# Kernel tuning notes

Hardware: AMD Instinct MI355X
Metric: run time of the kernel (lower is better)

The kernel has to match this reference:

```python
import jax, jax.numpy as jnp
import numpy as np

HEADS = 16
KV_HEADS = 4
DIM_HEAD = 64
DIM = 1024
B, N = 2, 2048


def setup_inputs() -> dict:
    key = jax.random.key(0)
    k1, k2, k3 = jax.random.split(key, 3)
    x = jax.random.normal(k1, (B, N, DIM), dtype=jnp.float32)
    Wq = jax.random.normal(k2, (DIM, HEADS * DIM_HEAD), dtype=jnp.float32) / np.sqrt(DIM)
    Wkv = jax.random.normal(k3, (DIM, 2 * KV_HEADS * DIM_HEAD), dtype=jnp.float32) / np.sqrt(DIM)
    k_scale = jnp.ones((HEADS, 1, DIM_HEAD), dtype=jnp.float32)
    return {"x": x, "Wq": Wq, "Wkv": Wkv, "k_scale": k_scale}


def reference(x, Wq, Wkv, k_scale):
    b, n, _ = x.shape
    g = HEADS // KV_HEADS  # query heads per kv head
    scale = DIM_HEAD ** -0.5
    # fused qkv projections (no bias)
    q = (x @ Wq).reshape(b, n, HEADS, DIM_HEAD)
    kv = x @ Wkv
    k, v = jnp.split(kv, 2, axis=-1)
    k = k.reshape(b, n, KV_HEADS, DIM_HEAD).transpose(0, 2, 1, 3)  # b k n d
    v = v.reshape(b, n, KV_HEADS, DIM_HEAD).transpose(0, 2, 1, 3)  # b k n d
    # group query heads: b, kv_heads, g, n, d
    qg = q.transpose(0, 2, 1, 3).reshape(b, KV_HEADS, g, n, DIM_HEAD)
    # per-query-head k scale, applied to the group-broadcast k (qk-norm)
    ks = k_scale.reshape(KV_HEADS, g, 1, DIM_HEAD)
    kk = k[:, :, None, :, :] * ks  # b k g n d
    dots = jnp.einsum('bkgid,bkgjd->bkgij', qg, kk) * scale
    attn = jax.nn.softmax(dots, axis=-1)
    out = jnp.einsum('bkgij,bkjd->bkgid', attn, v)  # v broadcast over g
    out = out.reshape(b, HEADS, n, DIM_HEAD).transpose(0, 2, 1, 3).reshape(b, n, HEADS * DIM_HEAD)
    return out
```

## Files before the change

kernel.cpp:

```cpp
#include <hip/hip_runtime.h>
#include <stdint.h>
#include <math.h>

typedef __attribute__((ext_vector_type(8))) __bf16 bf16x8;
typedef __attribute__((ext_vector_type(4))) float f32x4;
typedef __attribute__((ext_vector_type(16))) float f32x16;

__device__ __forceinline__ uint32_t f32_to_bf16_rne(float f) {
  union { float f; uint32_t u; } v; v.f = f;
  return (v.u + 0x7FFFu + ((v.u >> 16) & 1u)) >> 16;
}

__device__ __forceinline__ uint32_t cvt_pk_bf16(float lo, float hi) {
  uint32_t r;
  asm("v_cvt_pk_bf16_f32 %0, %1, %2" : "=v"(r) : "v"(lo), "v"(hi));
  return r;
}

__device__ __forceinline__ void gld16(void* lds, const void* g) {
  __builtin_amdgcn_global_load_lds(
      (__attribute__((address_space(1))) void*)(g),
      (__attribute__((address_space(3))) void*)(lds), 16, 0, 0);
}

__device__ __forceinline__ f32x4 mfma16(bf16x8 a, bf16x8 b, f32x4 c) {
  return __builtin_amdgcn_mfma_f32_16x16x32_bf16(a, b, c, 0, 0, 0);
}
__device__ __forceinline__ f32x16 mfma32(bf16x8 a, bf16x8 b, f32x16 c) {
  return __builtin_amdgcn_mfma_f32_32x32x16_bf16(a, b, c, 0, 0, 0);
}

#define LOG2E 1.44269504088896340736f

__global__ __launch_bounds__(256) void k_convert(const float* __restrict__ x,
                                                 const float* __restrict__ wq,
                                                 const float* __restrict__ wkv,
                                                 uint16_t* __restrict__ xb,
                                                 uint16_t* __restrict__ wt) {
  __shared__ float tile[64][65];
  int blk = blockIdx.x;
  int t = threadIdx.x;
  if (blk < 2048) {
    int i = blk * 256 + t;
    const float4* xv = (const float4*)x;
    float4 a = xv[2 * i], b2 = xv[2 * i + 1];
    uint32_t w0 = f32_to_bf16_rne(a.x) | (f32_to_bf16_rne(a.y) << 16);
    uint32_t w1 = f32_to_bf16_rne(a.z) | (f32_to_bf16_rne(a.w) << 16);
    uint32_t w2 = f32_to_bf16_rne(b2.x) | (f32_to_bf16_rne(b2.y) << 16);
    uint32_t w3 = f32_to_bf16_rne(b2.z) | (f32_to_bf16_rne(b2.w) << 16);
    ((uint4*)xb)[i] = make_uint4(w0, w1, w2, w3);
  } else {
    int blk2 = blk - 2048;
    int c0 = (blk2 % 24) * 64, k0 = (blk2 / 24) * 64;
    int col = t & 63, rq = t >> 6;
#pragma unroll
    for (int rr = 0; rr < 16; rr++) {
      int r = rr * 4 + rq;
      int c = c0 + col;
      float v = (c < 1024) ? wq[(uint64_t)(k0 + r) * 1024 + c]
                           : wkv[(uint64_t)(k0 + r) * 512 + (c - 1024)];
      tile[r][col] = v;
    }
    __syncthreads();
#pragma unroll
    for (int rr = 0; rr < 16; rr++) {
      int a = rr * 4 + rq;
      wt[(uint64_t)(c0 + a) * 1024 + k0 + col] = (uint16_t)f32_to_bf16_rne(tile[col][a]);
    }
  }
}

__global__ __launch_bounds__(256, 3) void k_proj_gemm(
    const uint16_t* __restrict__ xb, const uint16_t* __restrict__ wt,
    const float* __restrict__ kscale, uint16_t* __restrict__ q_ws,
    uint16_t* __restrict__ kf_ws, uint16_t* __restrict__ vf_ws) {
  __shared__ __align__(16) uint16_t ring[2][12288];
  int t = threadIdx.x;
  int w = t >> 6, l = t & 63;
  int lq = l & 15, lg = l >> 4;
  int id = blockIdx.x;
  int xcd = id & 7, idx = id >> 3;
  int rrp = idx & 3, cc = idx >> 2;
  int m0 = (xcd * 4 + rrp) * 128, n0 = cc * 64;
  int wr = w >> 1, wc = w & 1;
  f32x4 acc[4][2] = {};

  auto stage = [&](int slot, int k0) {
#pragma unroll
    for (int j = 0; j < 4; j++) {
      int c = j * 256 + t;
      int r = c >> 3, s = c & 7;
      int sl = s ^ (r & 7);
      gld16((char*)&ring[slot][0] + c * 16,
            xb + (uint64_t)(m0 + r) * 1024 + k0 + sl * 8);
    }
#pragma unroll
    for (int j = 0; j < 2; j++) {
      int c = j * 256 + t;
      int r = c >> 3, s = c & 7;
      int sl = s ^ (r & 7);
      gld16((char*)&ring[slot][8192] + c * 16,
            wt + (uint64_t)(n0 + r) * 1024 + k0 + sl * 8);
    }
  };

  stage(0, 0);
  asm volatile("s_waitcnt vmcnt(0)" ::: "memory");
  __builtin_amdgcn_s_barrier();

  int cur = 0;
  for (int it = 0; it < 16; ++it) {
    if (it + 1 < 16) stage(cur ^ 1, (it + 1) * 64);

    const uint16_t* As = &ring[cur][0];
    const uint16_t* Bs = &ring[cur][8192];
    bf16x8 af[2][4], bfr[2][2];
#pragma unroll
    for (int kk = 0; kk < 2; kk++) {
#pragma unroll
      for (int m = 0; m < 4; m++) {
        int r = wr * 64 + m * 16 + lq;
        int sl = (kk * 4 + lg) ^ (r & 7);
        af[kk][m] = *(const bf16x8*)(As + r * 64 + sl * 8);
      }
#pragma unroll
      for (int n = 0; n < 2; n++) {
        int r = wc * 32 + n * 16 + lq;
        int sl = (kk * 4 + lg) ^ (r & 7);
        bfr[kk][n] = *(const bf16x8*)(Bs + r * 64 + sl * 8);
      }
    }
    __builtin_amdgcn_s_setprio(1);
#pragma unroll
    for (int kk = 0; kk < 2; kk++)
#pragma unroll
      for (int m = 0; m < 4; m++)
#pragma unroll
        for (int n = 0; n < 2; n++)
          acc[m][n] = mfma16(af[kk][m], bfr[kk][n], acc[m][n]);
    __builtin_amdgcn_s_setprio(0);

    asm volatile("s_waitcnt vmcnt(0) lgkmcnt(0)" ::: "memory");
    __builtin_amdgcn_s_barrier();
    cur ^= 1;
  }

#pragma unroll
  for (int m = 0; m < 4; m++)
#pragma unroll
    for (int n = 0; n < 2; n++)
#pragma unroll
      for (int jj = 0; jj < 4; jj++) {
        int row = m0 + wr * 64 + m * 16 + 4 * lg + jj;
        int col = n0 + wc * 32 + n * 16 + lq;
        float val = acc[m][n][jj];
        int b = row >> 11, nn = row & 2047;
        if (col < 1024) {
          val *= kscale[col] * 0.125f * LOG2E;
          q_ws[((uint64_t)((b * 16 + (col >> 6)) * 2048 + nn)) * 64 + (col & 63)] =
              (uint16_t)f32_to_bf16_rne(val);
        } else if (col < 1280) {
          int kvh = (col - 1024) >> 6;
          int d = col & 63;
          int gsu = nn >> 5, lrr = nn & 31;
          int mm = d >> 4, hh = (d >> 3) & 1, el = d & 7;
          kf_ws[(uint64_t)(b * 4 + kvh) * 131072 +
                (uint64_t)((((gsu * 4 + mm) * 64) + hh * 32 + lrr) * 8 + el)] =
              (uint16_t)f32_to_bf16_rne(val);
        } else {
          int kvh = (col - 1280) >> 6;
          int d = col & 63;
          int gsu = nn >> 5, jj2 = (nn >> 4) & 1, hh = (nn >> 3) & 1, el = nn & 7;
          int dd = d >> 5, lrr = d & 31;
          vf_ws[(uint64_t)(b * 4 + kvh) * 131072 +
                (uint64_t)((((gsu * 4 + dd * 2 + jj2) * 64) + hh * 32 + lrr) * 8 + el)] =
              (uint16_t)f32_to_bf16_rne(val);
        }
      }
}

__global__ __launch_bounds__(512, 1) void k_attn(const uint16_t* __restrict__ q_ws,
                                                 const uint16_t* __restrict__ kf_ws,
                                                 const uint16_t* __restrict__ vf_ws,
                                                 float* __restrict__ out) {
  extern __shared__ __align__(16) char smem[];

  int t = threadIdx.x, w = t >> 6, l = t & 63;
  int lr = l & 31, hi = l >> 5;
  int qg = w & 3, half = w >> 2;
  int blk = blockIdx.x;
  int c = blk & 7, j = blk >> 3;
  int b = c >> 2, kvh = c & 3;
  int h = kvh * 4 + (j >> 3), qb = j & 7;

  const uint16_t* Qb = q_ws + (uint64_t)(b * 16 + h) * 2048 * 64;
  const uint16_t* Kb = kf_ws + (uint64_t)(b * 4 + kvh) * 131072;
  const uint16_t* Vb = vf_ws + (uint64_t)(b * 4 + kvh) * 131072;
  int qrow0 = qb * 256 + qg * 64;

  bf16x8 qfA[4], qfB[4];
#pragma unroll
  for (int m = 0; m < 4; m++) {
    qfA[m] = *(const bf16x8*)(Qb + (uint64_t)(qrow0 + lr) * 64 + m * 16 + hi * 8);
    qfB[m] = *(const bf16x8*)(Qb + (uint64_t)(qrow0 + 32 + lr) * 64 + m * 16 + hi * 8);
  }

  f32x16 oaccA[2] = {}, oaccB[2] = {};
  float lA = 0.f, lB = 0.f;

  const uint16_t* SbW = ((qg < 2) ? Kb : Vb) + (uint64_t)half * 65536 +
                        (uint64_t)((qg & 1) * 2) * 512 + l * 8;
  char* dstW = smem + half * 8192 + ((qg < 2) ? 0 : 4096) + (qg & 1) * 2048 + l * 16;

  auto stage = [&](int slot, int sul) {
    char* d = dstW + slot * 16384;
    const uint16_t* s = SbW + (uint64_t)sul * 2048;
    gld16(d, s);
    gld16(d + 1024, s + 512);
  };
  auto slotbase = [&](int slot) {
    return (const uint16_t*)(smem + slot * 16384 + half * 8192);
  };

  auto readK = [&](bf16x8* kf, const uint16_t* base) {
#pragma unroll
    for (int m = 0; m < 4; m++) kf[m] = *(const bf16x8*)(base + m * 512 + l * 8);
  };
  auto readV = [&](bf16x8* vf, const uint16_t* base) {
#pragma unroll
    for (int i = 0; i < 4; i++) vf[i] = *(const bf16x8*)(base + (4 + i) * 512 + l * 8);
  };
  auto qk = [&](const bf16x8* kf, const bf16x8* qf) {
    f32x16 T = {};
    __builtin_amdgcn_s_setprio(1);
#pragma unroll
    for (int m = 0; m < 4; m++) T = mfma32(kf[m], qf[m], T);
    __builtin_amdgcn_s_setprio(0);
    return T;
  };

  auto finish = [&](f32x16& Tc, const bf16x8* vf, f32x16* oacc, float& lsum) {
    float p[16];
#pragma unroll
    for (int e = 0; e < 16; e++) p[e] = __builtin_amdgcn_exp2f(Tc[e]);
    float sm0 = ((p[0] + p[1]) + (p[2] + p[3])) + ((p[4] + p[5]) + (p[6] + p[7]));
    float sm1 = ((p[8] + p[9]) + (p[10] + p[11])) + ((p[12] + p[13]) + (p[14] + p[15]));
    lsum += sm0 + sm1;

    bf16x8 pa[2];
#pragma unroll
    for (int jj = 0; jj < 2; jj++) {
      const float* pp = p + 8 * jj;
      uint32_t X = cvt_pk_bf16(pp[0], pp[1]);
      uint32_t Z = cvt_pk_bf16(pp[2], pp[3]);
      uint32_t Y = cvt_pk_bf16(pp[4], pp[5]);
      uint32_t W2 = cvt_pk_bf16(pp[6], pp[7]);
      asm volatile("v_permlane32_swap_b32 %0, %1" : "+v"(X), "+v"(Y));
      asm volatile("v_permlane32_swap_b32 %0, %1" : "+v"(Z), "+v"(W2));
      union { uint32_t u[4]; bf16x8 v; } pu;
      pu.u[0] = X; pu.u[1] = Z; pu.u[2] = Y; pu.u[3] = W2;
      pa[jj] = pu.v;
    }

    __builtin_amdgcn_s_setprio(1);
#pragma unroll
    for (int dd = 0; dd < 2; dd++)
#pragma unroll
      for (int jj = 0; jj < 2; jj++)
        oacc[dd] = mfma32(pa[jj], vf[dd * 2 + jj], oacc[dd]);
    __builtin_amdgcn_s_setprio(0);
  };

#pragma unroll
  for (int tt = 0; tt < 6; ++tt) stage(tt, tt);
  asm volatile("s_waitcnt vmcnt(4)" ::: "memory");
  __builtin_amdgcn_s_barrier();

  for (int iv = 0; iv < 16; ++iv) {
    int a = 2 * iv;
    int s0 = a + 6, s1 = a + 7;
    if (s0 > 31) s0 = 31;
    if (s1 > 31) s1 = 31;
    stage((a + 6) & 7, s0);
    stage((a + 7) & 7, s1);

    const uint16_t* b0 = slotbase(a & 7);
    const uint16_t* b1 = slotbase((a + 1) & 7);

    if (half == 0) {
      bf16x8 kf[4], vf[4];
      readK(kf, b0);
      readV(vf, b0);
      f32x16 Ta = qk(kf, qfA);
      f32x16 Tb = qk(kf, qfB);
      finish(Ta, vf, oaccA, lA);
      finish(Tb, vf, oaccB, lB);
      readK(kf, b1);
      readV(vf, b1);
      Ta = qk(kf, qfA);
      Tb = qk(kf, qfB);
      finish(Ta, vf, oaccA, lA);
      finish(Tb, vf, oaccB, lB);
    } else {
      bf16x8 kf0[4], kf1[4];
      readK(kf0, b0);
      readK(kf1, b1);
      f32x16 T0a = qk(kf0, qfA);
      f32x16 T0b = qk(kf0, qfB);
      f32x16 T1a = qk(kf1, qfA);
      f32x16 T1b = qk(kf1, qfB);
      bf16x8 vf[4];
      readV(vf, b0);
      finish(T0a, vf, oaccA, lA);
      finish(T0b, vf, oaccB, lB);
      readV(vf, b1);
      finish(T1a, vf, oaccA, lA);
      finish(T1b, vf, oaccB, lB);
    }

    asm volatile("s_waitcnt vmcnt(8)" ::: "memory");
    __builtin_amdgcn_s_barrier();
  }

  lA += __shfl_xor(lA, 32);
  lB += __shfl_xor(lB, 32);

  asm volatile("s_waitcnt vmcnt(0)" ::: "memory");
  __syncthreads();

  float* exch = (float*)smem;
  float* exl = (float*)(smem + 65536);
  if (half == 1) {
#pragma unroll
    for (int sub = 0; sub < 2; sub++) {
      f32x16* oacc = sub ? oaccB : oaccA;
#pragma unroll
      for (int r = 0; r < 16; r++) {
        int qr = (r & 3) + 8 * (r >> 2) + 4 * hi;
        exch[qg * 4096 + (sub * 32 + qr) * 64 + lr] = oacc[0][r];
        exch[qg * 4096 + (sub * 32 + qr) * 64 + 32 + lr] = oacc[1][r];
      }
    }
    if (hi == 0) {
      exl[qg * 64 + lr] = lA;
      exl[qg * 64 + 32 + lr] = lB;
    }
  }
  __syncthreads();
  if (half == 0) {
    lA += exl[qg * 64 + lr];
    lB += exl[qg * 64 + 32 + lr];
    float invA = 1.0f / lA, invB = 1.0f / lB;
#pragma unroll
    for (int sub = 0; sub < 2; sub++) {
      f32x16* oacc = sub ? oaccB : oaccA;
      float inv = sub ? invB : invA;
#pragma unroll
      for (int r = 0; r < 16; r++) {
        int qr = (r & 3) + 8 * (r >> 2) + 4 * hi;
        float iv = __shfl(inv, qr);
        float o0 = oacc[0][r] + exch[qg * 4096 + (sub * 32 + qr) * 64 + lr];
        float o1 = oacc[1][r] + exch[qg * 4096 + (sub * 32 + qr) * 64 + 32 + lr];
        float* orow =
            out + (uint64_t)(b * 2048 + qrow0 + sub * 32 + qr) * 1024 + h * 64 + lr;
        orow[0] = o0 * iv;
        orow[32] = o1 * iv;
      }
    }
  }
}

extern "C" void kernel_launch(void* const* d_in, const int* in_sizes, int n_in,
                              void* d_out, int out_size, void* d_ws, size_t ws_size,
                              hipStream_t stream) {
  const float* x = (const float*)d_in[0];
  const float* wq = (const float*)d_in[1];
  const float* wkv = (const float*)d_in[2];
  const float* kscale = (const float*)d_in[3];
  float* out = (float*)d_out;
  char* ws = (char*)d_ws;
  uint16_t* xb = (uint16_t*)(ws);
  uint16_t* wt = (uint16_t*)(ws + (8ull << 20));
  uint16_t* q_ws = (uint16_t*)(ws + (11ull << 20));
  uint16_t* kf_ws = (uint16_t*)(ws + (19ull << 20));
  uint16_t* vf_ws = (uint16_t*)(ws + (21ull << 20));

  static bool attr_set = false;
  if (!attr_set) {
    (void)hipFuncSetAttribute((const void*)k_attn,
                              hipFuncAttributeMaxDynamicSharedMemorySize, 131072);
    attr_set = true;
  }

  k_convert<<<2432, 256, 0, stream>>>(x, wq, wkv, xb, wt);
  k_proj_gemm<<<768, 256, 0, stream>>>(xb, wt, kscale, q_ws, kf_ws, vf_ws);
  k_attn<<<256, 512, 131072, stream>>>(q_ws, kf_ws, vf_ws, out);
}
```

Before: 69.62 us.

## Fuse x fp32-to-bf16 conversion into projection GEMM A-tile staging

```diff
diff --git a/kernel.cpp b/kernel.cpp
--- a/kernel.cpp
+++ b/kernel.cpp
@@ -32,46 +32,32 @@
 
 #define LOG2E 1.44269504088896340736f
 
-__global__ __launch_bounds__(256) void k_convert(const float* __restrict__ x,
-                                                 const float* __restrict__ wq,
-                                                 const float* __restrict__ wkv,
-                                                 uint16_t* __restrict__ xb,
-                                                 uint16_t* __restrict__ wt) {
+__global__ __launch_bounds__(256) void k_convert_w(const float* __restrict__ wq,
+                                                   const float* __restrict__ wkv,
+                                                   uint16_t* __restrict__ wt) {
   __shared__ float tile[64][65];
   int blk = blockIdx.x;
   int t = threadIdx.x;
-  if (blk < 2048) {
-    int i = blk * 256 + t;
-    const float4* xv = (const float4*)x;
-    float4 a = xv[2 * i], b2 = xv[2 * i + 1];
-    uint32_t w0 = f32_to_bf16_rne(a.x) | (f32_to_bf16_rne(a.y) << 16);
-    uint32_t w1 = f32_to_bf16_rne(a.z) | (f32_to_bf16_rne(a.w) << 16);
-    uint32_t w2 = f32_to_bf16_rne(b2.x) | (f32_to_bf16_rne(b2.y) << 16);
-    uint32_t w3 = f32_to_bf16_rne(b2.z) | (f32_to_bf16_rne(b2.w) << 16);
-    ((uint4*)xb)[i] = make_uint4(w0, w1, w2, w3);
-  } else {
-    int blk2 = blk - 2048;
-    int c0 = (blk2 % 24) * 64, k0 = (blk2 / 24) * 64;
-    int col = t & 63, rq = t >> 6;
-#pragma unroll
-    for (int rr = 0; rr < 16; rr++) {
-      int r = rr * 4 + rq;
-      int c = c0 + col;
-      float v = (c < 1024) ? wq[(uint64_t)(k0 + r) * 1024 + c]
-                           : wkv[(uint64_t)(k0 + r) * 512 + (c - 1024)];
-      tile[r][col] = v;
-    }
-    __syncthreads();
-#pragma unroll
-    for (int rr = 0; rr < 16; rr++) {
-      int a = rr * 4 + rq;
-      wt[(uint64_t)(c0 + a) * 1024 + k0 + col] = (uint16_t)f32_to_bf16_rne(tile[col][a]);
-    }
+  int c0 = (blk % 24) * 64, k0 = (blk / 24) * 64;
+  int col = t & 63, rq = t >> 6;
+#pragma unroll
+  for (int rr = 0; rr < 16; rr++) {
+    int r = rr * 4 + rq;
+    int c = c0 + col;
+    float v = (c < 1024) ? wq[(uint64_t)(k0 + r) * 1024 + c]
+                         : wkv[(uint64_t)(k0 + r) * 512 + (c - 1024)];
+    tile[r][col] = v;
+  }
+  __syncthreads();
+#pragma unroll
+  for (int rr = 0; rr < 16; rr++) {
+    int a = rr * 4 + rq;
+    wt[(uint64_t)(c0 + a) * 1024 + k0 + col] = (uint16_t)f32_to_bf16_rne(tile[col][a]);
   }
 }
 
 __global__ __launch_bounds__(256, 3) void k_proj_gemm(
-    const uint16_t* __restrict__ xb, const uint16_t* __restrict__ wt,
+    const float* __restrict__ x, const uint16_t* __restrict__ wt,
     const float* __restrict__ kscale, uint16_t* __restrict__ q_ws,
     uint16_t* __restrict__ kf_ws, uint16_t* __restrict__ vf_ws) {
   __shared__ __align__(16) uint16_t ring[2][12288];
@@ -85,15 +71,30 @@
   int wr = w >> 1, wc = w & 1;
   f32x4 acc[4][2] = {};
 
-  auto stage = [&](int slot, int k0) {
+  float4 ar[4][2];
+  auto loadA = [&](int k0) {
 #pragma unroll
     for (int j = 0; j < 4; j++) {
       int c = j * 256 + t;
       int r = c >> 3, s = c & 7;
       int sl = s ^ (r & 7);
-      gld16((char*)&ring[slot][0] + c * 16,
-            xb + (uint64_t)(m0 + r) * 1024 + k0 + sl * 8);
-    }
+      const float* src = x + (uint64_t)(m0 + r) * 1024 + k0 + sl * 8;
+      ar[j][0] = *(const float4*)(src);
+      ar[j][1] = *(const float4*)(src + 4);
+    }
+  };
+  auto writeA = [&](int slot) {
+#pragma unroll
+    for (int j = 0; j < 4; j++) {
+      int c = j * 256 + t;
+      uint32_t w0 = cvt_pk_bf16(ar[j][0].x, ar[j][0].y);
+      uint32_t w1 = cvt_pk_bf16(ar[j][0].z, ar[j][0].w);
+      uint32_t w2 = cvt_pk_bf16(ar[j][1].x, ar[j][1].y);
+      uint32_t w3 = cvt_pk_bf16(ar[j][1].z, ar[j][1].w);
+      *(uint4*)((char*)&ring[slot][0] + c * 16) = make_uint4(w0, w1, w2, w3);
+    }
+  };
+  auto stageB = [&](int slot, int k0) {
 #pragma unroll
     for (int j = 0; j < 2; j++) {
       int c = j * 256 + t;
@@ -104,13 +105,18 @@
     }
   };
 
-  stage(0, 0);
-  asm volatile("s_waitcnt vmcnt(0)" ::: "memory");
+  loadA(0);
+  stageB(0, 0);
+  writeA(0);
+  asm volatile("s_waitcnt vmcnt(0) lgkmcnt(0)" ::: "memory");
   __builtin_amdgcn_s_barrier();
 
   int cur = 0;
   for (int it = 0; it < 16; ++it) {
-    if (it + 1 < 16) stage(cur ^ 1, (it + 1) * 64);
+    if (it + 1 < 16) {
+      loadA((it + 1) * 64);
+      stageB(cur ^ 1, (it + 1) * 64);
+    }
 
     const uint16_t* As = &ring[cur][0];
     const uint16_t* Bs = &ring[cur][8192];
@@ -139,6 +145,8 @@
         for (int n = 0; n < 2; n++)
           acc[m][n] = mfma16(af[kk][m], bfr[kk][n], acc[m][n]);
     __builtin_amdgcn_s_setprio(0);
+
+    if (it + 1 < 16) writeA(cur ^ 1);
 
     asm volatile("s_waitcnt vmcnt(0) lgkmcnt(0)" ::: "memory");
     __builtin_amdgcn_s_barrier();
@@ -379,7 +387,6 @@
   const float* kscale = (const float*)d_in[3];
   float* out = (float*)d_out;
   char* ws = (char*)d_ws;
-  uint16_t* xb = (uint16_t*)(ws);
   uint16_t* wt = (uint16_t*)(ws + (8ull << 20));
   uint16_t* q_ws = (uint16_t*)(ws + (11ull << 20));
   uint16_t* kf_ws = (uint16_t*)(ws + (19ull << 20));
@@ -392,7 +399,7 @@
     attr_set = true;
   }
 
-  k_convert<<<2432, 256, 0, stream>>>(x, wq, wkv, xb, wt);
-  k_proj_gemm<<<768, 256, 0, stream>>>(xb, wt, kscale, q_ws, kf_ws, vf_ws);
+  k_convert_w<<<384, 256, 0, stream>>>(wq, wkv, wt);
+  k_proj_gemm<<<768, 256, 0, stream>>>(x, wt, kscale, q_ws, kf_ws, vf_ws);
   k_attn<<<256, 512, 131072, stream>>>(q_ws, kf_ws, vf_ws, out);
 }
```

Result: slower. 76.82 us (+10.3%).
